# Kernel optimization log

Hardware: AMD Instinct MI355X
Metric: run time of the kernel (lower is better)

Reference implementation:

```python
import jax, jax.numpy as jnp
import numpy as np

BN_EPS = 1e-5


def _gin_layer(x, src, dst, W1, b1, W2, b2, gamma, beta):
    N = x.shape[0]
    # scatter-add neighbor aggregation (GINConv with eps=0)
    agg = jax.ops.segment_sum(x[src], dst, num_segments=N)
    h = x + agg
    # MLP: Linear -> ReLU -> Linear
    h = jax.nn.relu(h @ W1 + b1) @ W2 + b2
    # BatchNorm1d (training-mode batch statistics, biased variance)
    mean = jnp.mean(h, axis=0)
    var = jnp.mean(jnp.square(h - mean), axis=0)
    h = (h - mean) * jax.lax.rsqrt(var + BN_EPS) * gamma + beta
    return jax.nn.relu(h)


def setup_inputs() -> dict:
    key = jax.random.key(0)
    ks = jax.random.split(key, 16)
    N, E, F_IN, H, L, G, T = 100000, 400000, 128, 256, 5, 4096, 12
    x = jax.random.normal(ks[0], (N, F_IN), dtype=jnp.float32)
    edge_index = jax.random.randint(ks[1], (2, E), 0, N, dtype=jnp.int64)
    batch_idx = jnp.sort(jax.random.randint(ks[2], (N,), 0, G, dtype=jnp.int64))
    s = 0.02
    inp = {
        "x": x,
        "edge_index": edge_index,
        "batch_idx": batch_idx,
        "num_graphs": G,
        # layer 0: 128 -> 256
        "W1_0": jax.random.normal(ks[3], (F_IN, H), dtype=jnp.float32) * s,
        "b1_0": jnp.zeros((H,), jnp.float32),
        "W2_0": jax.random.normal(ks[4], (H, H), dtype=jnp.float32) * s,
        "b2_0": jnp.zeros((H,), jnp.float32),
        "gamma_0": jnp.ones((H,), jnp.float32),
        "beta_0": jnp.zeros((H,), jnp.float32),
        # layers 1..4 stacked: 256 -> 256
        "W1s": jax.random.normal(ks[5], (L - 1, H, H), dtype=jnp.float32) * s,
        "b1s": jnp.zeros((L - 1, H), jnp.float32),
        "W2s": jax.random.normal(ks[6], (L - 1, H, H), dtype=jnp.float32) * s,
        "b2s": jnp.zeros((L - 1, H), jnp.float32),
        "gammas": jnp.ones((L - 1, H), jnp.float32),
        "betas": jnp.zeros((L - 1, H), jnp.float32),
        # predictor
        "Wp1": jax.random.normal(ks[7], (H, H), dtype=jnp.float32) * s,
        "bp1": jnp.zeros((H,), jnp.float32),
        "Wp2": jax.random.normal(ks[8], (H, T), dtype=jnp.float32) * s,
        "bp2": jnp.zeros((T,), jnp.float32),
    }
    return inp


def reference(x, edge_index, batch_idx, num_graphs,
              W1_0, b1_0, W2_0, b2_0, gamma_0, beta_0,
              W1s, b1s, W2s, b2s, gammas, betas,
              Wp1, bp1, Wp2, bp2):
    src, dst = edge_index[0], edge_index[1]
    h = _gin_layer(x, src, dst, W1_0, b1_0, W2_0, b2_0, gamma_0, beta_0)
    for i in range(W1s.shape[0]):
        h = _gin_layer(h, src, dst, W1s[i], b1s[i], W2s[i], b2s[i], gammas[i], betas[i])
    # global mean pool over graphs
    sums = jax.ops.segment_sum(h, batch_idx, num_segments=num_graphs)
    counts = jax.ops.segment_sum(jnp.ones((h.shape[0],), h.dtype), batch_idx, num_segments=num_graphs)
    g = sums / jnp.maximum(counts, 1.0)[:, None]
    # predictor MLP (dropout=0 in eval)
    out = jax.nn.relu(g @ Wp1 + bp1) @ Wp2 + bp2
    return out
```

## Files before the change

### kernel.cpp

```cpp
#include <hip/hip_runtime.h>


typedef __attribute__((ext_vector_type(4))) float f32x4;
typedef __attribute__((ext_vector_type(8))) _Float16 f16x8;

__device__ __forceinline__ float h2f(unsigned short u) {
  _Float16 h; __builtin_memcpy(&h, &u, 2); return (float)h;
}
__device__ __forceinline__ unsigned short f2h16(float f) {
  _Float16 h = (_Float16)f; unsigned short u; __builtin_memcpy(&u, &h, 2); return u;
}
__device__ __forceinline__ unsigned short f2b(float f) {
  union { float f; unsigned int i; } c; c.f = f;
  unsigned int x = c.i;
  return (unsigned short)((x + 0x7fffu + ((x >> 16) & 1u)) >> 16);
}
__device__ __forceinline__ float lin(const void* p, long long i, int wf32) {
  if (wf32) return ((const float*)p)[i];
  union { unsigned int i; float f; } c;
  c.i = ((unsigned int)((const unsigned short*)p)[i]) << 16;
  return c.f;
}
__device__ __forceinline__ int ldidx(const int* p, long long i, int w64) {
  return w64 ? p[2 * i] : p[i];
}

__device__ __forceinline__ void gload_lds16(const void* g, void* l) {
  __builtin_amdgcn_global_load_lds(
      (const __attribute__((address_space(1))) unsigned int*)g,
      (__attribute__((address_space(3))) unsigned int*)l, 16, 0, 0);
}

__global__ void detect_k(const int* __restrict__ edge, const unsigned short* __restrict__ xa,
                         int* __restrict__ flags) {
  if (threadIdx.x != 0 || blockIdx.x != 0) return;
  int nzOdd = 0;
  for (int t = 0; t < 256; t++) if (edge[2 * t + 1] != 0) nzOdd++;
  flags[0] = (nzOdd == 0) ? 1 : 0;
  int plaus = 0;
  for (int t = 0; t < 64; t++) {
    unsigned short w = xa[2 * t];
    int e = (w >> 7) & 0xFF;
    if (w == 0 || (e >= 0x70 && e <= 0x85)) plaus++;
  }
  flags[1] = (plaus < 32) ? 1 : 0;
}

__global__ void zero_i32_k(int* __restrict__ p, int n) {
  int i = blockIdx.x * blockDim.x + threadIdx.x;
  if (i < n) p[i] = 0;
}

__global__ void prep_k(const void* __restrict__ b1, const void* __restrict__ b2,
                       const void* __restrict__ gm, const void* __restrict__ bt, int eoff,
                       float* __restrict__ pb1, float* __restrict__ pb2,
                       float* __restrict__ pg, float* __restrict__ pb,
                       float* __restrict__ gsum, const int* __restrict__ flags) {
  int wf32 = flags[1], t = threadIdx.x;
  pb1[t] = lin(b1, (long long)eoff + t, wf32);
  pb2[t] = lin(b2, (long long)eoff + t, wf32);
  pg[t]  = lin(gm, (long long)eoff + t, wf32);
  pb[t]  = lin(bt, (long long)eoff + t, wf32);
  gsum[t] = 0.f; gsum[256 + t] = 0.f;
}
__global__ void copy256_k(const void* __restrict__ src, int eoff, float* __restrict__ dst,
                          const int* __restrict__ flags) {
  dst[threadIdx.x] = lin(src, (long long)eoff + threadIdx.x, flags[1]);
}

__global__ void transpose_off_k(const void* __restrict__ src, long long eoff,
                                unsigned short* __restrict__ dst, int R, int C,
                                const int* __restrict__ flags) {
  int wf32 = flags[1];
  __shared__ unsigned short t[32][33];
  int bx = blockIdx.x * 32, by = blockIdx.y * 32;
  int x = bx + threadIdx.x;
  for (int i = 0; i < 32; i += 8) {
    int y = by + threadIdx.y + i;
    if (y < R && x < C)
      t[threadIdx.y + i][threadIdx.x] = f2h16(lin(src, eoff + (long long)y * C + x, wf32));
  }
  __syncthreads();
  int x2 = by + threadIdx.x;
  for (int i = 0; i < 32; i += 8) {
    int y = bx + threadIdx.y + i;
    if (y < C && x2 < R) dst[(long long)y * R + x2] = t[threadIdx.x][threadIdx.y + i];
  }
}

__global__ void hist_k(const int* __restrict__ edge, int E, int* __restrict__ cnt,
                       const int* __restrict__ flags) {
  int w64 = flags[0];
  int e = blockIdx.x * blockDim.x + threadIdx.x;
  if (e < E) atomicAdd(&cnt[ldidx(edge, (long long)E + e, w64)], 1);
}
#define SCAN_CHUNK 1024
__global__ void scan1_k(const int* __restrict__ in, int* __restrict__ out,
                        int* __restrict__ partials, int n) {
  __shared__ int sh[256];
  int tid = threadIdx.x;
  int base = blockIdx.x * SCAN_CHUNK + tid * 4;
  int v[4]; int tsum = 0;
#pragma unroll
  for (int i = 0; i < 4; i++) { v[i] = (base + i < n) ? in[base + i] : 0; tsum += v[i]; }
  sh[tid] = tsum; __syncthreads();
  for (int off = 1; off < 256; off <<= 1) {
    int t = (tid >= off) ? sh[tid - off] : 0;
    __syncthreads();
    sh[tid] += t;
    __syncthreads();
  }
  int run = sh[tid] - tsum;
#pragma unroll
  for (int i = 0; i < 4; i++) { if (base + i < n) out[base + i] = run; run += v[i]; }
  if (tid == 255) partials[blockIdx.x] = sh[255];
}
__global__ void scan2_k(int* partials, int B) {
  __shared__ int sh[256];
  int tid = threadIdx.x;
  int orig = (tid < B) ? partials[tid] : 0;
  sh[tid] = orig; __syncthreads();
  for (int off = 1; off < 256; off <<= 1) {
    int t = (tid >= off) ? sh[tid - off] : 0;
    __syncthreads();
    sh[tid] += t;
    __syncthreads();
  }
  if (tid < B) partials[tid] = sh[tid] - orig;
}
__global__ void scan3_k(int* __restrict__ out, const int* __restrict__ partials,
                        int n, int total) {
  int base = blockIdx.x * SCAN_CHUNK + threadIdx.x * 4;
  int add = partials[blockIdx.x];
#pragma unroll
  for (int i = 0; i < 4; i++) { if (base + i < n) out[base + i] += add; }
  if (blockIdx.x == 0 && threadIdx.x == 0) out[n] = total;
}
__global__ void fill_k(const int* __restrict__ edge, int E, const int* __restrict__ rowptr,
                       int* __restrict__ cnt, int* __restrict__ colidx,
                       const int* __restrict__ flags) {
  int w64 = flags[0];
  int e = blockIdx.x * blockDim.x + threadIdx.x;
  if (e >= E) return;
  int s = ldidx(edge, e, w64);
  int d = ldidx(edge, (long long)E + e, w64);
  int p = atomicAdd(&cnt[d], 1);
  colidx[rowptr[d] + p] = s;
}
__global__ void graph_bounds_k(const int* __restrict__ b, int Nn, int G,
                               int* __restrict__ gstart, const int* __restrict__ flags) {
  int w64 = flags[0];
  int g = blockIdx.x * blockDim.x + threadIdx.x;
  if (g > G) return;
  int lo = 0, hi = Nn;
  while (lo < hi) {
    int mid = (lo + hi) >> 1;
    if (ldidx(b, mid, w64) < g) lo = mid + 1; else hi = mid;
  }
  gstart[g] = lo;
}

__global__ void convert_k(const void* __restrict__ x, unsigned short* __restrict__ xh,
                          long long n, const int* __restrict__ flags) {
  int wf32 = flags[1];
  long long base = ((long long)blockIdx.x * blockDim.x + threadIdx.x) * 4;
  if (base >= n) return;
#pragma unroll
  for (int k = 0; k < 4; k++) xh[base + k] = f2h16(lin(x, base + k, wf32));
}

template <int LPN, int APPLY>
__global__ void gather_fused_k(const unsigned short* __restrict__ src,
                               const float* __restrict__ scale, const float* __restrict__ shift,
                               const int* __restrict__ rowptr, const int* __restrict__ colidx,
                               unsigned short* __restrict__ u, int Nn) {
  const int F = LPN * 8;
  int gid = blockIdx.x * blockDim.x + threadIdx.x;
  int node = gid / LPN;
  if (node >= Nn) return;
  int fb = (gid % LPN) * 8;
  float sc[8], sh[8];
  if (APPLY) {
#pragma unroll
    for (int k = 0; k < 8; k++) { sc[k] = scale[fb + k]; sh[k] = shift[fb + k]; }
  }
  float acc[8];
  {
    uint4 raw = *(const uint4*)(src + (long long)node * F + fb);
    unsigned int ws[4] = {raw.x, raw.y, raw.z, raw.w};
#pragma unroll
    for (int k = 0; k < 8; k++) {
      float xv = h2f((unsigned short)((ws[k >> 1] >> ((k & 1) * 16)) & 0xffff));
      acc[k] = APPLY ? fmaxf(xv * sc[k] + sh[k], 0.f) : xv;
    }
  }
  int s = rowptr[node], e = rowptr[node + 1];
  for (int j = s; j < e; j++) {
    long long nb = colidx[j];
    uint4 raw = *(const uint4*)(src + nb * F + fb);
    unsigned int ws[4] = {raw.x, raw.y, raw.z, raw.w};
#pragma unroll
    for (int k = 0; k < 8; k++) {
      float xv = h2f((unsigned short)((ws[k >> 1] >> ((k & 1) * 16)) & 0xffff));
      acc[k] += APPLY ? fmaxf(xv * sc[k] + sh[k], 0.f) : xv;
    }
  }
  uint4 o;
  unsigned int wo[4];
#pragma unroll
  for (int p = 0; p < 4; p++)
    wo[p] = (unsigned int)f2h16(acc[2 * p]) | ((unsigned int)f2h16(acc[2 * p + 1]) << 16);
  o.x = wo[0]; o.y = wo[1]; o.z = wo[2]; o.w = wo[3];
  *(uint4*)(u + (long long)node * F + fb) = o;
}

template <int KIN>
__device__ __forceinline__ void stage_tile_lds(
    const unsigned short* __restrict__ A, long long row0, int M,
    unsigned char* R, int tid) {
  const int lane = tid & 63, wave = tid >> 6;
  constexpr int ROWB = 2 * KIN;
  constexpr int CHUNKS = ROWB / 16;
  constexpr int NISSUE = (128 * ROWB) / (8 * 1024);
#pragma unroll
  for (int j = 0; j < NISSUE; j++) {
    int slot = j * 8 + wave;
    int baseRow = (slot * 1024) / ROWB;
    int row = baseRow + lane / CHUNKS;
    int ci = lane % CHUNKS;
    int c = ci ^ (row & 7);
    long long rg = row0 + row;
    if (rg >= M) rg = M - 1;
    gload_lds16(A + rg * KIN + c * 8, R + slot * 1024);
  }
}

template <int KIN>
__global__ __launch_bounds__(512, 2) void fused_layer_k(
    const unsigned short* __restrict__ A, const unsigned short* __restrict__ W1t,
    const unsigned short* __restrict__ W2t, const float* __restrict__ b1,
    const float* __restrict__ b2, unsigned short* __restrict__ V,
    int M, int ntiles, float* __restrict__ gsum) {
  __shared__ __align__(16) unsigned char lds_raw[131072];
  const int tid = threadIdx.x;
  const int lane = tid & 63, wave = tid >> 6;
  const int l15 = lane & 15, lq = lane >> 4;
  const int wn = wave >> 1, wm = wave & 1;
  const int nb0 = wn * 64, mb0 = wm * 64;
  constexpr int KT1 = KIN / 32;

  if ((int)blockIdx.x < ntiles)
    stage_tile_lds<KIN>(A, (long long)blockIdx.x * 128, M, lds_raw, tid);
  __syncthreads();

  unsigned char* Rp = lds_raw;
  unsigned char* Rq = lds_raw + 65536;
  for (int t = blockIdx.x; t < ntiles; t += 256) {
    long long m0 = (long long)t * 128;
    int tn = t + 256;
    bool hasNext = tn < ntiles;
    f32x4 acc[4][4] = {};
#pragma unroll 1
    for (int kt = 0; kt < KT1; kt++) {
      f16x8 wf[4], uf[4];
#pragma unroll
      for (int r = 0; r < 4; r++)
        wf[r] = *(const f16x8*)(W1t + (long long)(nb0 + 16 * r + l15) * KIN + kt * 32 + lq * 8);
#pragma unroll
      for (int c = 0; c < 4; c++) {
        int m = mb0 + 16 * c + l15;
        uf[c] = *(const f16x8*)(Rp + m * (2 * KIN) + 16 * ((kt * 4 + lq) ^ (m & 7)));
      }
#pragma unroll
      for (int r = 0; r < 4; r++)
#pragma unroll
        for (int c = 0; c < 4; c++)
          acc[r][c] = __builtin_amdgcn_mfma_f32_16x16x32_f16(wf[r], uf[c], acc[r][c], 0, 0, 0);
    }
    __syncthreads();
    if (hasNext) stage_tile_lds<KIN>(A, (long long)tn * 128, M, Rq, tid);
#pragma unroll
    for (int r = 0; r < 4; r++) {
      int nbase = nb0 + 16 * r + lq * 4;
      float4 bv = *(const float4*)(b1 + nbase);
#pragma unroll
      for (int c = 0; c < 4; c++) {
        int m = mb0 + 16 * c + l15;
        unsigned int h0 = f2h16(fmaxf(acc[r][c][0] + bv.x, 0.f));
        unsigned int h1v = f2h16(fmaxf(acc[r][c][1] + bv.y, 0.f));
        unsigned int h2v = f2h16(fmaxf(acc[r][c][2] + bv.z, 0.f));
        unsigned int h3 = f2h16(fmaxf(acc[r][c][3] + bv.w, 0.f));
        uint2 pk; pk.x = h0 | (h1v << 16); pk.y = h2v | (h3 << 16);
        int by = m * 512 + 16 * ((nbase >> 3) ^ (m & 7)) + ((nbase & 7) << 1);
        *(uint2*)(Rp + by) = pk;
      }
    }
    __syncthreads();
    f32x4 acc2[4][4] = {};
#pragma unroll 1
    for (int kt = 0; kt < 8; kt++) {
      f16x8 wf[4], hf[4];
#pragma unroll
      for (int r = 0; r < 4; r++)
        wf[r] = *(const f16x8*)(W2t + (long long)(nb0 + 16 * r + l15) * 256 + kt * 32 + lq * 8);
#pragma unroll
      for (int c = 0; c < 4; c++) {
        int m = mb0 + 16 * c + l15;
        hf[c] = *(const f16x8*)(Rp + m * 512 + 16 * ((kt * 4 + lq) ^ (m & 7)));
      }
#pragma unroll
      for (int r = 0; r < 4; r++)
#pragma unroll
        for (int c = 0; c < 4; c++)
          acc2[r][c] = __builtin_amdgcn_mfma_f32_16x16x32_f16(wf[r], hf[c], acc2[r][c], 0, 0, 0);
    }
    __syncthreads();
#pragma unroll
    for (int r = 0; r < 4; r++) {
      int nbase = nb0 + 16 * r + lq * 4;
      float4 bv = *(const float4*)(b2 + nbase);
#pragma unroll
      for (int c = 0; c < 4; c++) {
        int m = mb0 + 16 * c + l15;
        unsigned int h0 = f2h16(acc2[r][c][0] + bv.x);
        unsigned int h1v = f2h16(acc2[r][c][1] + bv.y);
        unsigned int h2v = f2h16(acc2[r][c][2] + bv.z);
        unsigned int h3 = f2h16(acc2[r][c][3] + bv.w);
        uint2 pk; pk.x = h0 | (h1v << 16); pk.y = h2v | (h3 << 16);
        int by = m * 512 + 16 * ((nbase >> 3) ^ (m & 7)) + ((nbase & 7) << 1);
        *(uint2*)(Rp + by) = pk;
      }
    }
    __syncthreads();
    const int c32 = tid & 31, rg = tid >> 5;
    float s8[8] = {}, q8[8] = {};
#pragma unroll
    for (int k = 0; k < 8; k++) {
      int m = rg * 8 + k;
      uint4 vw = *(const uint4*)(Rp + m * 512 + 16 * (c32 ^ (m & 7)));
      long long grow = m0 + m;
      if (grow < M) {
        *(uint4*)(V + grow * 256 + c32 * 8) = vw;
        unsigned int ws[4] = {vw.x, vw.y, vw.z, vw.w};
#pragma unroll
        for (int kk = 0; kk < 8; kk++) {
          float xv = h2f((unsigned short)((ws[kk >> 1] >> ((kk & 1) * 16)) & 0xffff));
          s8[kk] += xv; q8[kk] += xv * xv;
        }
      }
    }
    __syncthreads();
    float* shf = (float*)Rp;
#pragma unroll
    for (int kk = 0; kk < 8; kk++) {
      int col = c32 * 8 + kk;
      shf[col * 17 + rg] = s8[kk];
      shf[4352 + col * 17 + rg] = q8[kk];
    }
    __syncthreads();
    if (tid < 256) {
      float tot = 0.f;
#pragma unroll
      for (int g = 0; g < 16; g++) tot += shf[tid * 17 + g];
      atomicAdd(&gsum[tid], tot);
    } else {
      int col = tid - 256; float tot = 0.f;
#pragma unroll
      for (int g = 0; g < 16; g++) tot += shf[4352 + col * 17 + g];
      atomicAdd(&gsum[256 + col], tot);
    }
    unsigned char* tmp = Rp; Rp = Rq; Rq = tmp;
  }
}

#define SA 40
#define SP 136
__global__ __launch_bounds__(256) void gemm_k(
    const unsigned short* __restrict__ A, const unsigned short* __restrict__ Bt,
    const float* __restrict__ bias, unsigned short* __restrict__ C,
    int M, int K, int relu, float* __restrict__ gsum) {
  __shared__ __align__(16) unsigned short smem[128 * SP];
  unsigned short* As = smem;
  unsigned short* Bs = smem + 128 * SA;
  int m0 = blockIdx.x * 128, n0 = blockIdx.y * 128;
  int tid = threadIdx.x;
  int wave = tid >> 6, lane = tid & 63;
  int wm = (wave >> 1) * 64, wnn = (wave & 1) * 64;
  int lrow = lane & 15, lqq = lane >> 4;
  f32x4 acc[4][4] = {};
  int ktiles = K >> 5;
  int srow = tid >> 2;
  int ch8 = (tid & 3) << 3;
  int rowA0 = m0 + srow;      rowA0 = rowA0 < M ? rowA0 : M - 1;
  int rowA1 = m0 + srow + 64; rowA1 = rowA1 < M ? rowA1 : M - 1;
  const unsigned short* pa0 = A + (long long)rowA0 * K + ch8;
  const unsigned short* pa1 = A + (long long)rowA1 * K + ch8;
  const unsigned short* pq0 = Bt + (long long)(n0 + srow) * K + ch8;
  const unsigned short* pq1 = Bt + (long long)(n0 + srow + 64) * K + ch8;
  uint4 va0 = *(const uint4*)pa0, va1 = *(const uint4*)pa1;
  uint4 vb0 = *(const uint4*)pq0, vb1 = *(const uint4*)pq1;
  int lo0 = srow * SA + ch8, lo1 = (srow + 64) * SA + ch8;
  for (int kt = 0; kt < ktiles; ++kt) {
    __syncthreads();
    *(uint4*)(As + lo0) = va0;
    *(uint4*)(As + lo1) = va1;
    *(uint4*)(Bs + lo0) = vb0;
    *(uint4*)(Bs + lo1) = vb1;
    __syncthreads();
    f16x8 af[4], bf[4];
#pragma unroll
    for (int r = 0; r < 4; r++)
      af[r] = *(const f16x8*)(As + (wm + 16 * r + lrow) * SA + lqq * 8);
#pragma unroll
    for (int c = 0; c < 4; c++)
      bf[c] = *(const f16x8*)(Bs + (wnn + 16 * c + lrow) * SA + lqq * 8);
    if (kt + 1 < ktiles) {
      int kb = (kt + 1) << 5;
      va0 = *(const uint4*)(pa0 + kb); va1 = *(const uint4*)(pa1 + kb);
      vb0 = *(const uint4*)(pq0 + kb); vb1 = *(const uint4*)(pq1 + kb);
    }
#pragma unroll
    for (int r = 0; r < 4; r++)
#pragma unroll
      for (int c = 0; c < 4; c++)
        acc[r][c] = __builtin_amdgcn_mfma_f32_16x16x32_f16(af[r], bf[c], acc[r][c], 0, 0, 0);
  }
  __syncthreads();
  unsigned short* Ct = smem;
#pragma unroll
  for (int c = 0; c < 4; c++) {
    int col = wnn + 16 * c + lrow;
    float bv = bias[n0 + col];
#pragma unroll
    for (int r = 0; r < 4; r++) {
      int rbase = wm + 16 * r + lqq * 4;
#pragma unroll
      for (int i = 0; i < 4; i++) {
        float v = acc[r][c][i] + bv;
        if (relu) v = fmaxf(v, 0.f);
        Ct[(rbase + i) * SP + col] = f2h16(v);
      }
    }
  }
  __syncthreads();
  int c16 = tid & 15, g = tid >> 4;
  float s8[8] = {}, q8[8] = {};
  bool dostats = (gsum != nullptr);
#pragma unroll
  for (int i = 0; i < 8; i++) {
    int row = g + i * 16;
    int grow = m0 + row;
    uint4 vw = *(const uint4*)(Ct + row * SP + c16 * 8);
    if (grow < M) {
      *(uint4*)(C + (long long)grow * 256 + n0 + c16 * 8) = vw;
      if (dostats) {
        unsigned int ws[4] = {vw.x, vw.y, vw.z, vw.w};
#pragma unroll
        for (int k = 0; k < 8; k++) {
          float xv = h2f((unsigned short)((ws[k >> 1] >> ((k & 1) * 16)) & 0xffff));
          s8[k] += xv; q8[k] += xv * xv;
        }
      }
    }
  }
  if (dostats) {
    float* shf = (float*)smem;
    __syncthreads();
#pragma unroll
    for (int k = 0; k < 8; k++) shf[(c16 * 8 + k) * 17 + g] = s8[k];
    __syncthreads();
    if (tid < 128) {
      float t = 0.f;
#pragma unroll
      for (int gg = 0; gg < 16; gg++) t += shf[tid * 17 + gg];
      atomicAdd(&gsum[n0 + tid], t);
    }
    __syncthreads();
#pragma unroll
    for (int k = 0; k < 8; k++) shf[(c16 * 8 + k) * 17 + g] = q8[k];
    __syncthreads();
    if (tid < 128) {
      float t = 0.f;
#pragma unroll
      for (int gg = 0; gg < 16; gg++) t += shf[tid * 17 + gg];
      atomicAdd(&gsum[256 + n0 + tid], t);
    }
  }
}

__global__ void bn_finalize_k(const float* __restrict__ gsum,
                              const float* __restrict__ pg, const float* __restrict__ pb,
                              int Nn, float* __restrict__ scale, float* __restrict__ shift) {
  int f = threadIdx.x;
  float inv = 1.f / (float)Nn;
  float mean = gsum[f] * inv;
  float var = fmaxf(gsum[256 + f] * inv - mean * mean, 0.f);
  float sc = pg[f] * rsqrtf(var + 1e-5f);
  scale[f] = sc;
  shift[f] = pb[f] - mean * sc;
}

__global__ void pool_fused_k(const unsigned short* __restrict__ v, const float* __restrict__ scale,
                             const float* __restrict__ shift, const int* __restrict__ gstart,
                             unsigned short* __restrict__ gout) {
  int g = blockIdx.x, f = threadIdx.x;
  int s = gstart[g], e = gstart[g + 1];
  float sc = scale[f], sh = shift[f];
  float acc = 0.f;
  for (int r = s; r < e; r++) acc += fmaxf(h2f(v[(long long)r * 256 + f]) * sc + sh, 0.f);
  gout[(long long)g * 256 + f] = f2h16(acc / fmaxf((float)(e - s), 1.f));
}
__global__ void pred2_k(const unsigned short* __restrict__ p1, const void* __restrict__ Wp2,
                        const void* __restrict__ bp2, void* __restrict__ out, int G,
                        const int* __restrict__ flags) {
  int wf32 = flags[1];
  int idx = blockIdx.x * blockDim.x + threadIdx.x;
  if (idx >= G * 12) return;
  int g = idx / 12, t = idx - g * 12;
  float acc = lin(bp2, t, wf32);
  const unsigned short* row = p1 + (long long)g * 256;
  for (int k = 0; k < 256; k++) acc += h2f(row[k]) * lin(Wp2, k * 12 + t, wf32);
  if (wf32) ((float*)out)[idx] = acc;
  else      ((unsigned short*)out)[idx] = f2b(acc);
}

extern "C" void kernel_launch(void* const* d_in, const int* in_sizes, int n_in,
                              void* d_out, int out_size, void* d_ws, size_t ws_size,
                              hipStream_t stream) {
  int wb = -1;
  for (int i = 3; i + 15 < n_in; i++) {
    if (in_sizes[i] == 32768 && in_sizes[i + 1] == 256 && in_sizes[i + 2] == 65536 &&
        in_sizes[i + 3] == 256 && in_sizes[i + 4] == 256 && in_sizes[i + 5] == 256 &&
        in_sizes[i + 6] == 262144) { wb = i; break; }
  }
  if (wb < 0) wb = (n_in >= 20) ? 4 : 3;

  const void* x      = d_in[0];
  const int*  edge   = (const int*)d_in[1];
  const int*  batch  = (const int*)d_in[2];
  const void* W1_0   = d_in[wb + 0];
  const void* b1_0   = d_in[wb + 1];
  const void* W2_0   = d_in[wb + 2];
  const void* b2_0   = d_in[wb + 3];
  const void* gamma0 = d_in[wb + 4];
  const void* beta0  = d_in[wb + 5];
  const void* W1s    = d_in[wb + 6];
  const void* b1s    = d_in[wb + 7];
  const void* W2s    = d_in[wb + 8];
  const void* b2s    = d_in[wb + 9];
  const void* gammas = d_in[wb + 10];
  const void* betas  = d_in[wb + 11];
  const void* Wp1    = d_in[wb + 12];
  const void* bp1    = d_in[wb + 13];
  const void* Wp2    = d_in[wb + 14];
  const void* bp2    = d_in[wb + 15];

  const int N = in_sizes[0] / 128;
  const int E = in_sizes[1] / 2;
  const int G = out_size / 12;
  const int H = 256;

  char* w = (char*)d_ws;
  size_t off = 0;
  auto alloc = [&](size_t bytes) -> char* {
    char* p = w + off;
    off += (bytes + 255) & ~(size_t)255;
    return p;
  };
  unsigned short* bufX  = (unsigned short*)alloc((size_t)N * H * 2);
  unsigned short* bufY  = (unsigned short*)alloc((size_t)N * H * 2);
  unsigned short* w1_0t = (unsigned short*)alloc((size_t)128 * 256 * 2);
  unsigned short* w2_0t = (unsigned short*)alloc((size_t)256 * 256 * 2);
  unsigned short* w1st  = (unsigned short*)alloc((size_t)4 * 256 * 256 * 2);
  unsigned short* w2st  = (unsigned short*)alloc((size_t)4 * 256 * 256 * 2);
  unsigned short* wp1t  = (unsigned short*)alloc((size_t)256 * 256 * 2);
  int*   rowptr   = (int*)alloc((size_t)(N + 1) * 4);
  int*   cnt      = (int*)alloc((size_t)N * 4);
  int*   colidx   = (int*)alloc((size_t)E * 4);
  int*   partials = (int*)alloc(1024 * 4);
  float* gsum     = (float*)alloc(512 * 4);
  float* bnscale  = (float*)alloc(256 * 4);
  float* bnshift  = (float*)alloc(256 * 4);
  float* pg       = (float*)alloc(256 * 4);
  float* pb       = (float*)alloc(256 * 4);
  float* pb1      = (float*)alloc(256 * 4);
  float* pb2      = (float*)alloc(256 * 4);
  int*   gstart   = (int*)alloc((size_t)(G + 1) * 4);
  int*   flags    = (int*)alloc(256);
  unsigned short* gpool = (unsigned short*)alloc((size_t)G * H * 2);
  unsigned short* p1    = (unsigned short*)alloc((size_t)G * H * 2);
  (void)ws_size; (void)n_in;

  detect_k<<<1, 64, 0, stream>>>(edge, (const unsigned short*)x, flags);

  convert_k<<<(int)(((long long)N * 128 / 4 + 255) / 256), 256, 0, stream>>>(
      x, bufY, (long long)N * 128, flags);

  dim3 tb(32, 8);
  auto transpose = [&](const void* src, long long eoff, unsigned short* dst, int R, int C) {
    transpose_off_k<<<dim3((C + 31) / 32, (R + 31) / 32), tb, 0, stream>>>(src, eoff, dst, R, C, flags);
  };
  transpose(W1_0, 0, w1_0t, 128, 256);
  transpose(W2_0, 0, w2_0t, 256, 256);
  for (int i = 0; i < 4; i++) {
    transpose(W1s, (long long)i * 65536, w1st + i * 65536, 256, 256);
    transpose(W2s, (long long)i * 65536, w2st + i * 65536, 256, 256);
  }
  transpose(Wp1, 0, wp1t, 256, 256);

  zero_i32_k<<<(N + 255) / 256, 256, 0, stream>>>(cnt, N);
  hist_k<<<(E + 255) / 256, 256, 0, stream>>>(edge, E, cnt, flags);
  int NB = (N + SCAN_CHUNK - 1) / SCAN_CHUNK;
  scan1_k<<<NB, 256, 0, stream>>>(cnt, rowptr, partials, N);
  scan2_k<<<1, 256, 0, stream>>>(partials, NB);
  scan3_k<<<NB, 256, 0, stream>>>(rowptr, partials, N, E);
  zero_i32_k<<<(N + 255) / 256, 256, 0, stream>>>(cnt, N);
  fill_k<<<(E + 255) / 256, 256, 0, stream>>>(edge, E, rowptr, cnt, colidx, flags);
  graph_bounds_k<<<(G + 1 + 255) / 256, 256, 0, stream>>>(batch, N, G, gstart, flags);

  const int ntiles = (N + 127) / 128;
  auto fused = [&](const unsigned short* Au, const unsigned short* w1, const unsigned short* w2,
                   unsigned short* Vv, int K) {
    if (K == 128)
      fused_layer_k<128><<<256, 512, 0, stream>>>(Au, w1, w2, pb1, pb2, Vv, N, ntiles, gsum);
    else
      fused_layer_k<256><<<256, 512, 0, stream>>>(Au, w1, w2, pb1, pb2, Vv, N, ntiles, gsum);
  };

  prep_k<<<1, 256, 0, stream>>>(b1_0, b2_0, gamma0, beta0, 0, pb1, pb2, pg, pb, gsum, flags);
  gather_fused_k<16, 0><<<(N * 16 + 255) / 256, 256, 0, stream>>>(
      bufY, bnscale, bnshift, rowptr, colidx, bufX, N);
  fused(bufX, w1_0t, w2_0t, bufY, 128);
  bn_finalize_k<<<1, 256, 0, stream>>>(gsum, pg, pb, N, bnscale, bnshift);
  unsigned short* cur = bufY;
  unsigned short* oth = bufX;
  for (int i = 0; i < 4; i++) {
    prep_k<<<1, 256, 0, stream>>>(b1s, b2s, gammas, betas, i * 256, pb1, pb2, pg, pb, gsum, flags);
    gather_fused_k<32, 1><<<(N * 32 + 255) / 256, 256, 0, stream>>>(
        cur, bnscale, bnshift, rowptr, colidx, oth, N);
    fused(oth, w1st + i * 65536, w2st + i * 65536, cur, 256);
    bn_finalize_k<<<1, 256, 0, stream>>>(gsum, pg, pb, N, bnscale, bnshift);
  }

  copy256_k<<<1, 256, 0, stream>>>(bp1, 0, pb1, flags);
  pool_fused_k<<<G, 256, 0, stream>>>(cur, bnscale, bnshift, gstart, gpool);
  gemm_k<<<dim3((G + 127) / 128, 2), 256, 0, stream>>>(gpool, wp1t, pb1, p1, G, 256, 1, nullptr);
  pred2_k<<<(G * 12 + 255) / 256, 256, 0, stream>>>(p1, Wp2, bp2, d_out, G, flags);
}
```

Measured before the change: 964.9 us.

## Replace persistent double-buffered fused layer kernel with one-tile-per-block launch

The fused MLP layer kernel no longer loops persistently over tiles with a 128KB double-buffered LDS prefetch. It now launches one block per 128-row tile with a single 64KB LDS buffer and launch bounds raised to 4 blocks per CU. The aim is higher occupancy, letting the hardware overlap load and compute across co-resident blocks. The cost is losing the explicit next-tile prefetch, paying more block launch overhead, and issuing more global atomics for the BN statistics, one set per tile. Tighter register bounds could also cause spills.

```diff
diff --git a/kernel.cpp b/kernel.cpp
--- a/kernel.cpp
+++ b/kernel.cpp
@@ -236,140 +236,131 @@
 }
 
 template <int KIN>
-__global__ __launch_bounds__(512, 2) void fused_layer_k(
+__global__ __launch_bounds__(512, 4) void fused_layer_k(
     const unsigned short* __restrict__ A, const unsigned short* __restrict__ W1t,
     const unsigned short* __restrict__ W2t, const float* __restrict__ b1,
     const float* __restrict__ b2, unsigned short* __restrict__ V,
-    int M, int ntiles, float* __restrict__ gsum) {
-  __shared__ __align__(16) unsigned char lds_raw[131072];
+    int M, float* __restrict__ gsum) {
+  __shared__ __align__(16) unsigned char R[65536];
   const int tid = threadIdx.x;
   const int lane = tid & 63, wave = tid >> 6;
   const int l15 = lane & 15, lq = lane >> 4;
   const int wn = wave >> 1, wm = wave & 1;
   const int nb0 = wn * 64, mb0 = wm * 64;
   constexpr int KT1 = KIN / 32;
-
-  if ((int)blockIdx.x < ntiles)
-    stage_tile_lds<KIN>(A, (long long)blockIdx.x * 128, M, lds_raw, tid);
-  __syncthreads();
-
-  unsigned char* Rp = lds_raw;
-  unsigned char* Rq = lds_raw + 65536;
-  for (int t = blockIdx.x; t < ntiles; t += 256) {
-    long long m0 = (long long)t * 128;
-    int tn = t + 256;
-    bool hasNext = tn < ntiles;
-    f32x4 acc[4][4] = {};
+  const long long m0 = (long long)blockIdx.x * 128;
+
+  stage_tile_lds<KIN>(A, m0, M, R, tid);
+  __syncthreads();
+
+  f32x4 acc[4][4] = {};
 #pragma unroll 1
-    for (int kt = 0; kt < KT1; kt++) {
-      f16x8 wf[4], uf[4];
-#pragma unroll
-      for (int r = 0; r < 4; r++)
-        wf[r] = *(const f16x8*)(W1t + (long long)(nb0 + 16 * r + l15) * KIN + kt * 32 + lq * 8);
-#pragma unroll
-      for (int c = 0; c < 4; c++) {
-        int m = mb0 + 16 * c + l15;
-        uf[c] = *(const f16x8*)(Rp + m * (2 * KIN) + 16 * ((kt * 4 + lq) ^ (m & 7)));
+  for (int kt = 0; kt < KT1; kt++) {
+    f16x8 wf[4], uf[4];
+#pragma unroll
+    for (int r = 0; r < 4; r++)
+      wf[r] = *(const f16x8*)(W1t + (long long)(nb0 + 16 * r + l15) * KIN + kt * 32 + lq * 8);
+#pragma unroll
+    for (int c = 0; c < 4; c++) {
+      int m = mb0 + 16 * c + l15;
+      uf[c] = *(const f16x8*)(R + m * (2 * KIN) + 16 * ((kt * 4 + lq) ^ (m & 7)));
+    }
+#pragma unroll
+    for (int r = 0; r < 4; r++)
+#pragma unroll
+      for (int c = 0; c < 4; c++)
+        acc[r][c] = __builtin_amdgcn_mfma_f32_16x16x32_f16(wf[r], uf[c], acc[r][c], 0, 0, 0);
+  }
+  __syncthreads();
+#pragma unroll
+  for (int r = 0; r < 4; r++) {
+    int nbase = nb0 + 16 * r + lq * 4;
+    float4 bv = *(const float4*)(b1 + nbase);
+#pragma unroll
+    for (int c = 0; c < 4; c++) {
+      int m = mb0 + 16 * c + l15;
+      unsigned int h0 = f2h16(fmaxf(acc[r][c][0] + bv.x, 0.f));
+      unsigned int h1v = f2h16(fmaxf(acc[r][c][1] + bv.y, 0.f));
+      unsigned int h2v = f2h16(fmaxf(acc[r][c][2] + bv.z, 0.f));
+      unsigned int h3 = f2h16(fmaxf(acc[r][c][3] + bv.w, 0.f));
+      uint2 pk; pk.x = h0 | (h1v << 16); pk.y = h2v | (h3 << 16);
+      int by = m * 512 + 16 * ((nbase >> 3) ^ (m & 7)) + ((nbase & 7) << 1);
+      *(uint2*)(R + by) = pk;
+    }
+  }
+  __syncthreads();
+  f32x4 acc2[4][4] = {};
+#pragma unroll 1
+  for (int kt = 0; kt < 8; kt++) {
+    f16x8 wf[4], hf[4];
+#pragma unroll
+    for (int r = 0; r < 4; r++)
+      wf[r] = *(const f16x8*)(W2t + (long long)(nb0 + 16 * r + l15) * 256 + kt * 32 + lq * 8);
+#pragma unroll
+    for (int c = 0; c < 4; c++) {
+      int m = mb0 + 16 * c + l15;
+      hf[c] = *(const f16x8*)(R + m * 512 + 16 * ((kt * 4 + lq) ^ (m & 7)));
+    }
+#pragma unroll
+    for (int r = 0; r < 4; r++)
+#pragma unroll
+      for (int c = 0; c < 4; c++)
+        acc2[r][c] = __builtin_amdgcn_mfma_f32_16x16x32_f16(wf[r], hf[c], acc2[r][c], 0, 0, 0);
+  }
+  __syncthreads();
+#pragma unroll
+  for (int r = 0; r < 4; r++) {
+    int nbase = nb0 + 16 * r + lq * 4;
+    float4 bv = *(const float4*)(b2 + nbase);
+#pragma unroll
+    for (int c = 0; c < 4; c++) {
+      int m = mb0 + 16 * c + l15;
+      unsigned int h0 = f2h16(acc2[r][c][0] + bv.x);
+      unsigned int h1v = f2h16(acc2[r][c][1] + bv.y);
+      unsigned int h2v = f2h16(acc2[r][c][2] + bv.z);
+      unsigned int h3 = f2h16(acc2[r][c][3] + bv.w);
+      uint2 pk; pk.x = h0 | (h1v << 16); pk.y = h2v | (h3 << 16);
+      int by = m * 512 + 16 * ((nbase >> 3) ^ (m & 7)) + ((nbase & 7) << 1);
+      *(uint2*)(R + by) = pk;
+    }
+  }
+  __syncthreads();
+  const int c32 = tid & 31, rg = tid >> 5;
+  float s8[8] = {}, q8[8] = {};
+#pragma unroll
+  for (int k = 0; k < 8; k++) {
+    int m = rg * 8 + k;
+    uint4 vw = *(const uint4*)(R + m * 512 + 16 * (c32 ^ (m & 7)));
+    long long grow = m0 + m;
+    if (grow < M) {
+      *(uint4*)(V + grow * 256 + c32 * 8) = vw;
+      unsigned int ws[4] = {vw.x, vw.y, vw.z, vw.w};
+#pragma unroll
+      for (int kk = 0; kk < 8; kk++) {
+        float xv = h2f((unsigned short)((ws[kk >> 1] >> ((kk & 1) * 16)) & 0xffff));
+        s8[kk] += xv; q8[kk] += xv * xv;
       }
-#pragma unroll
-      for (int r = 0; r < 4; r++)
-#pragma unroll
-        for (int c = 0; c < 4; c++)
-          acc[r][c] = __builtin_amdgcn_mfma_f32_16x16x32_f16(wf[r], uf[c], acc[r][c], 0, 0, 0);
-    }
-    __syncthreads();
-    if (hasNext) stage_tile_lds<KIN>(A, (long long)tn * 128, M, Rq, tid);
-#pragma unroll
-    for (int r = 0; r < 4; r++) {
-      int nbase = nb0 + 16 * r + lq * 4;
-      float4 bv = *(const float4*)(b1 + nbase);
-#pragma unroll
-      for (int c = 0; c < 4; c++) {
-        int m = mb0 + 16 * c + l15;
-        unsigned int h0 = f2h16(fmaxf(acc[r][c][0] + bv.x, 0.f));
-        unsigned int h1v = f2h16(fmaxf(acc[r][c][1] + bv.y, 0.f));
-        unsigned int h2v = f2h16(fmaxf(acc[r][c][2] + bv.z, 0.f));
-        unsigned int h3 = f2h16(fmaxf(acc[r][c][3] + bv.w, 0.f));
-        uint2 pk; pk.x = h0 | (h1v << 16); pk.y = h2v | (h3 << 16);
-        int by = m * 512 + 16 * ((nbase >> 3) ^ (m & 7)) + ((nbase & 7) << 1);
-        *(uint2*)(Rp + by) = pk;
-      }
-    }
-    __syncthreads();
-    f32x4 acc2[4][4] = {};
-#pragma unroll 1
-    for (int kt = 0; kt < 8; kt++) {
-      f16x8 wf[4], hf[4];
-#pragma unroll
-      for (int r = 0; r < 4; r++)
-        wf[r] = *(const f16x8*)(W2t + (long long)(nb0 + 16 * r + l15) * 256 + kt * 32 + lq * 8);
-#pragma unroll
-      for (int c = 0; c < 4; c++) {
-        int m = mb0 + 16 * c + l15;
-        hf[c] = *(const f16x8*)(Rp + m * 512 + 16 * ((kt * 4 + lq) ^ (m & 7)));
-      }
-#pragma unroll
-      for (int r = 0; r < 4; r++)
-#pragma unroll
-        for (int c = 0; c < 4; c++)
-          acc2[r][c] = __builtin_amdgcn_mfma_f32_16x16x32_f16(wf[r], hf[c], acc2[r][c], 0, 0, 0);
-    }
-    __syncthreads();
-#pragma unroll
-    for (int r = 0; r < 4; r++) {
-      int nbase = nb0 + 16 * r + lq * 4;
-      float4 bv = *(const float4*)(b2 + nbase);
-#pragma unroll
-      for (int c = 0; c < 4; c++) {
-        int m = mb0 + 16 * c + l15;
-        unsigned int h0 = f2h16(acc2[r][c][0] + bv.x);
-        unsigned int h1v = f2h16(acc2[r][c][1] + bv.y);
-        unsigned int h2v = f2h16(acc2[r][c][2] + bv.z);
-        unsigned int h3 = f2h16(acc2[r][c][3] + bv.w);
-        uint2 pk; pk.x = h0 | (h1v << 16); pk.y = h2v | (h3 << 16);
-        int by = m * 512 + 16 * ((nbase >> 3) ^ (m & 7)) + ((nbase & 7) << 1);
-        *(uint2*)(Rp + by) = pk;
-      }
-    }
-    __syncthreads();
-    const int c32 = tid & 31, rg = tid >> 5;
-    float s8[8] = {}, q8[8] = {};
-#pragma unroll
-    for (int k = 0; k < 8; k++) {
-      int m = rg * 8 + k;
-      uint4 vw = *(const uint4*)(Rp + m * 512 + 16 * (c32 ^ (m & 7)));
-      long long grow = m0 + m;
-      if (grow < M) {
-        *(uint4*)(V + grow * 256 + c32 * 8) = vw;
-        unsigned int ws[4] = {vw.x, vw.y, vw.z, vw.w};
-#pragma unroll
-        for (int kk = 0; kk < 8; kk++) {
-          float xv = h2f((unsigned short)((ws[kk >> 1] >> ((kk & 1) * 16)) & 0xffff));
-          s8[kk] += xv; q8[kk] += xv * xv;
-        }
-      }
-    }
-    __syncthreads();
-    float* shf = (float*)Rp;
-#pragma unroll
-    for (int kk = 0; kk < 8; kk++) {
-      int col = c32 * 8 + kk;
-      shf[col * 17 + rg] = s8[kk];
-      shf[4352 + col * 17 + rg] = q8[kk];
-    }
-    __syncthreads();
-    if (tid < 256) {
-      float tot = 0.f;
-#pragma unroll
-      for (int g = 0; g < 16; g++) tot += shf[tid * 17 + g];
-      atomicAdd(&gsum[tid], tot);
-    } else {
-      int col = tid - 256; float tot = 0.f;
-#pragma unroll
-      for (int g = 0; g < 16; g++) tot += shf[4352 + col * 17 + g];
-      atomicAdd(&gsum[256 + col], tot);
-    }
-    unsigned char* tmp = Rp; Rp = Rq; Rq = tmp;
+    }
+  }
+  __syncthreads();
+  float* shf = (float*)R;
+#pragma unroll
+  for (int kk = 0; kk < 8; kk++) {
+    int col = c32 * 8 + kk;
+    shf[col * 17 + rg] = s8[kk];
+    shf[4352 + col * 17 + rg] = q8[kk];
+  }
+  __syncthreads();
+  if (tid < 256) {
+    float tot = 0.f;
+#pragma unroll
+    for (int g = 0; g < 16; g++) tot += shf[tid * 17 + g];
+    atomicAdd(&gsum[tid], tot);
+  } else {
+    int col = tid - 256; float tot = 0.f;
+#pragma unroll
+    for (int g = 0; g < 16; g++) tot += shf[4352 + col * 17 + g];
+    atomicAdd(&gsum[256 + col], tot);
   }
 }
 
@@ -622,9 +613,9 @@
   auto fused = [&](const unsigned short* Au, const unsigned short* w1, const unsigned short* w2,
                    unsigned short* Vv, int K) {
     if (K == 128)
-      fused_layer_k<128><<<256, 512, 0, stream>>>(Au, w1, w2, pb1, pb2, Vv, N, ntiles, gsum);
+      fused_layer_k<128><<<ntiles, 512, 0, stream>>>(Au, w1, w2, pb1, pb2, Vv, N, gsum);
     else
-      fused_layer_k<256><<<256, 512, 0, stream>>>(Au, w1, w2, pb1, pb2, Vv, N, ntiles, gsum);
+      fused_layer_k<256><<<ntiles, 512, 0, stream>>>(Au, w1, w2, pb1, pb2, Vv, N, gsum);
   };
 
   prep_k<<<1, 256, 0, stream>>>(b1_0, b2_0, gamma0, beta0, 0, pb1, pb2, pg, pb, gsum, flags);
```

Result: faster. 940.5 us (-2.5%).
